# Optimization experiments

Measured on AMD Instinct MI355X. Metric: run time of the kernel, lower is better.

Reference implementation:

```python
import jax, jax.numpy as jnp
import numpy as np

SFREQ = 250.0
L_FREQ, H_FREQ = 4.0, 8.0
N_TAPS = 413  # odd, zero-phase FIR


def _bandpass_fir(numtaps, lf, hf, sfreq):
    # Hamming-windowed sinc band-pass (firwin-style), matching MNE's fir_design='firwin' spirit
    n = np.arange(numtaps) - (numtaps - 1) / 2.0
    lp = lambda fc: (2.0 * fc / sfreq) * np.sinc(2.0 * fc / sfreq * n)
    h = (lp(hf) - lp(lf)) * np.hamming(numtaps)
    return h.astype(np.float32)


def setup_inputs() -> dict:
    key = jax.random.key(0)
    x = jax.random.normal(key, (64, 64, 10000), dtype=jnp.float32)
    h = jnp.asarray(_bandpass_fir(N_TAPS, L_FREQ, H_FREQ, SFREQ))
    return {"x": x, "h": h}


def reference(x, h):
    # x: [B, C, T], h: [n_h] FIR filter. Equivalent math to _overlap_add_filter:
    # reflect_limited padding + full linear FFT convolution + zero-phase crop.
    T = x.shape[-1]
    n_h = h.shape[0]
    n_edge = min(n_h, T) - 1
    # reflect_limited pad: 2*x[0] - x[n_edge:0:-1] (left), 2*x[-1] - x[-2:-n_edge-2:-1] (right)
    left = 2.0 * x[..., :1] - x[..., 1:n_edge + 1][..., ::-1]
    right = 2.0 * x[..., -1:] - x[..., -n_edge - 1:-1][..., ::-1]
    x_ext = jnp.concatenate([left, x, right], axis=-1)  # [B, C, T + 2*n_edge]
    n_x = T + 2 * n_edge
    n_full = n_x + n_h - 1
    n_fft = 1 << (n_full - 1).bit_length()  # single big FFT == overlap-add result
    Xf = jnp.fft.rfft(x_ext, n_fft)
    Hf = jnp.fft.rfft(h.astype(x_ext.dtype), n_fft)
    y = jnp.fft.irfft(Xf * Hf, n_fft)  # full linear convolution of x_ext with h
    shift = (n_h - 1) // 2 + n_edge  # zero-phase delay compensation + edge crop
    return jax.lax.dynamic_slice_in_dim(y, shift, T, axis=-1).astype(x.dtype)
```

## Files before the change

kernel.cpp:

```cpp
#include <hip/hip_runtime.h>


#define T_LEN 10000
#define N_H   413
#define SHIFT 206
#define CB    512
#define NSEG  20
#define ROWH  936
#define NQ    28
#define AROWL 472

typedef _Float16 v8h   __attribute__((ext_vector_type(8)));
typedef float    v16f  __attribute__((ext_vector_type(16)));
typedef float    v4f   __attribute__((ext_vector_type(4)));
typedef float    f32x2 __attribute__((ext_vector_type(2)));

__device__ __forceinline__ void store_col(float* __restrict__ orow, const v16f& acc,
                                          int tbase, int guard_needed) {
    #pragma unroll
    for (int g = 0; g < 4; ++g) {
        if (!guard_needed || (tbase + 8 * g) < T_LEN) {
            *(v4f*)(orow + 8 * g) =
                (v4f){acc[4*g], acc[4*g+1], acc[4*g+2], acc[4*g+3]};
        }
    }
}

__global__ __launch_bounds__(256, 3) void FilterBank_20624432955781_kernel(
    const float* __restrict__ x, const float* __restrict__ h, float* __restrict__ out) {
    __shared__ alignas(16) _Float16 lds_e[16 * ROWH];
    __shared__ alignas(16) _Float16 arow[2][8][AROWL];

    const int tid = threadIdx.x;
    const int t0b = blockIdx.x * CB;
    const int r0  = blockIdx.y * 16;

    for (int z = tid; z < 8 * AROWL; z += 256) {
        const int r = z / AROWL, vv = z - r * AROWL;
        const int idx = 436 + r - vv;
        const float gv = (idx >= 0 && idx < N_H) ? h[idx] : 0.0f;
        const _Float16 hi = (_Float16)gv;
        arow[0][r][vv] = hi;
        arow[1][r][vv] = (_Float16)(gv - (float)hi);
    }

    {
        const int rr = tid >> 4;
        const int jt = tid & 15;
        const float* __restrict__ xr = x + (size_t)(r0 + rr) * T_LEN;
        _Float16* __restrict__ erow = lds_e + rr * ROWH;
        #pragma unroll
        for (int it = 0; it < 4; ++it) {
            const int c = jt + 16 * it;
            if (c < 58) {
                const int j0 = t0b + 16 * c;
                float v[16];
                if (j0 >= SHIFT && j0 + 16 <= T_LEN + SHIFT) {
                    const f32x2* xp = (const f32x2*)(xr + (j0 - SHIFT));
                    #pragma unroll
                    for (int p = 0; p < 8; ++p) { f32x2 t2 = xp[p]; v[2*p] = t2.x; v[2*p+1] = t2.y; }
                } else {
                    #pragma unroll
                    for (int k = 0; k < 16; ++k) {
                        const int j = j0 + k;
                        if (j < SHIFT)              v[k] = 2.0f * xr[0] - xr[SHIFT - j];
                        else if (j < T_LEN + SHIFT) v[k] = xr[j - SHIFT];
                        else                        v[k] = 2.0f * xr[T_LEN - 1] - xr[2 * T_LEN + SHIFT - 2 - j];
                    }
                }
                v8h h0, h1;
                #pragma unroll
                for (int k = 0; k < 8; ++k) { h0[k] = (_Float16)v[k]; h1[k] = (_Float16)v[8 + k]; }
                *(v8h*)(erow + 16 * c)     = h0;
                *(v8h*)(erow + 16 * c + 8) = h1;
            }
        }
    }
    __syncthreads();

    const int l  = tid & 63;
    const int wv = tid >> 6;
    const int n  = l & 31;
    const int hh = l >> 5;
    const int ch = n & 15;
    const int th = n >> 4;
    const int vv0 = 24 + 8 * hh - 8 * (n >> 3);
    const v8h* __restrict__ pah = (const v8h*)(&arow[0][n & 7][0] + vv0);
    const v8h* __restrict__ pal = (const v8h*)(&arow[1][n & 7][0] + vv0);
    const _Float16* __restrict__ ebase = lds_e + ch * ROWH + 32 * th + 8 * hh;

    const int n_out = T_LEN - t0b;
    const int NP = (n_out < CB ? n_out + 63 : CB + 63) >> 6;
    const int guard = (t0b + CB > T_LEN);

    int p = wv;
    if (p + 4 < NP) {
        const _Float16* __restrict__ eb0 = ebase + 64 * p;
        const _Float16* __restrict__ eb1 = ebase + 64 * (p + 4);
        v16f acc0 = (v16f)(0.0f), acc1 = (v16f)(0.0f);
        #pragma unroll
        for (int q = 0; q < NQ; ++q) {
            const v8h ah = pah[2 * q];
            const v8h al = pal[2 * q];
            const v8h b0 = *(const v8h*)(eb0 + 16 * q);
            const v8h b1 = *(const v8h*)(eb1 + 16 * q);
            acc0 = __builtin_amdgcn_mfma_f32_32x32x16_f16(ah, b0, acc0, 0, 0, 0);
            acc1 = __builtin_amdgcn_mfma_f32_32x32x16_f16(ah, b1, acc1, 0, 0, 0);
            acc0 = __builtin_amdgcn_mfma_f32_32x32x16_f16(al, b0, acc0, 0, 0, 0);
            acc1 = __builtin_amdgcn_mfma_f32_32x32x16_f16(al, b1, acc1, 0, 0, 0);
        }
        {
            const int tb0 = t0b + 64 * p + 32 * th + 4 * hh;
            const int tb1 = t0b + 64 * (p + 4) + 32 * th + 4 * hh;
            float* orow = out + (size_t)(r0 + ch) * T_LEN;
            store_col(orow + tb0, acc0, tb0, guard);
            store_col(orow + tb1, acc1, tb1, guard);
        }
        p += 8;
    }
    for (; p < NP; p += 4) {
        const _Float16* __restrict__ eb0 = ebase + 64 * p;
        v16f acc0 = (v16f)(0.0f);
        #pragma unroll
        for (int q = 0; q < NQ; ++q) {
            const v8h ah = pah[2 * q];
            const v8h al = pal[2 * q];
            const v8h b0 = *(const v8h*)(eb0 + 16 * q);
            acc0 = __builtin_amdgcn_mfma_f32_32x32x16_f16(ah, b0, acc0, 0, 0, 0);
            acc0 = __builtin_amdgcn_mfma_f32_32x32x16_f16(al, b0, acc0, 0, 0, 0);
        }
        const int tb0 = t0b + 64 * p + 32 * th + 4 * hh;
        store_col(out + (size_t)(r0 + ch) * T_LEN + tb0, acc0, tb0, guard);
    }
}

extern "C" void kernel_launch(void* const* d_in, const int* in_sizes, int n_in,
                              void* d_out, int out_size, void* d_ws, size_t ws_size,
                              hipStream_t stream) {
    const float* x = (const float*)d_in[0];
    const float* h = (const float*)d_in[1];
    float* out = (float*)d_out;
    dim3 grid(NSEG, 64 * 64 / 16);
    FilterBank_20624432955781_kernel<<<grid, dim3(256), 0, stream>>>(x, h, out);
}
```

Measured before the change: 374.0 us.

## Loop each block over seven segments and prefetch the next input into registers

Each block now processes up to seven consecutive 512-sample segments of its 16 rows instead of one, so the grid shrinks from 20 to 3 column blocks. The fp16 filter Toeplitz table is built once per block instead of once per segment. While the MFMAs run on the current segment, the next segment's input is loaded into registers, then converted and written to LDS between two barriers. MFMA sections also raise wave priority with s_setprio. In exchange there are fewer blocks, more register pressure from the 64-float staging buffer, two extra barriers per segment, and full MFMA work on the partial tail segment.

```diff
diff --git a/kernel.cpp b/kernel.cpp
--- a/kernel.cpp
+++ b/kernel.cpp
@@ -5,7 +5,7 @@
 #define N_H   413
 #define SHIFT 206
 #define CB    512
-#define NSEG  20
+#define BSPAN 3584
 #define ROWH  936
 #define NQ    28
 #define AROWL 472
@@ -14,6 +14,51 @@
 typedef float    v16f  __attribute__((ext_vector_type(16)));
 typedef float    v4f   __attribute__((ext_vector_type(4)));
 typedef float    f32x2 __attribute__((ext_vector_type(2)));
+
+__device__ __forceinline__ void stage_load(const float* __restrict__ xr, int t0s,
+                                           int jt, float sv[4][16]) {
+    #pragma unroll
+    for (int it = 0; it < 4; ++it) {
+        const int c = jt + 16 * it;
+        if (c < 58) {
+            const int j0 = t0s + 16 * c;
+            if (j0 >= SHIFT && j0 + 16 <= T_LEN + SHIFT) {
+                const f32x2* xp = (const f32x2*)(xr + (j0 - SHIFT));
+                #pragma unroll
+                for (int p = 0; p < 8; ++p) {
+                    f32x2 t2 = xp[p]; sv[it][2*p] = t2.x; sv[it][2*p+1] = t2.y;
+                }
+            } else {
+                #pragma unroll
+                for (int k = 0; k < 16; ++k) {
+                    const int j = j0 + k;
+                    float v;
+                    if (j < SHIFT)              v = 2.0f * xr[0] - xr[SHIFT - j];
+                    else if (j < T_LEN + SHIFT) v = xr[j - SHIFT];
+                    else                        v = 2.0f * xr[T_LEN - 1] - xr[2 * T_LEN + SHIFT - 2 - j];
+                    sv[it][k] = v;
+                }
+            }
+        }
+    }
+}
+
+__device__ __forceinline__ void stage_write(_Float16* __restrict__ erow, int jt,
+                                            const float sv[4][16]) {
+    #pragma unroll
+    for (int it = 0; it < 4; ++it) {
+        const int c = jt + 16 * it;
+        if (c < 58) {
+            v8h h0, h1;
+            #pragma unroll
+            for (int k = 0; k < 8; ++k) {
+                h0[k] = (_Float16)sv[it][k]; h1[k] = (_Float16)sv[it][8 + k];
+            }
+            *(v8h*)(erow + 16 * c)     = h0;
+            *(v8h*)(erow + 16 * c + 8) = h1;
+        }
+    }
+}
 
 __device__ __forceinline__ void store_col(float* __restrict__ orow, const v16f& acc,
                                           int tbase, int guard_needed) {
@@ -31,9 +76,10 @@
     __shared__ alignas(16) _Float16 lds_e[16 * ROWH];
     __shared__ alignas(16) _Float16 arow[2][8][AROWL];
 
-    const int tid = threadIdx.x;
-    const int t0b = blockIdx.x * CB;
-    const int r0  = blockIdx.y * 16;
+    const int tid    = threadIdx.x;
+    const int t_base = blockIdx.x * BSPAN;
+    const int r0     = blockIdx.y * 16;
+    const int nseg   = min(7, (T_LEN - t_base + CB - 1) / CB);
 
     for (int z = tid; z < 8 * AROWL; z += 256) {
         const int r = z / AROWL, vv = z - r * AROWL;
@@ -44,38 +90,14 @@
         arow[1][r][vv] = (_Float16)(gv - (float)hi);
     }
 
-    {
-        const int rr = tid >> 4;
-        const int jt = tid & 15;
-        const float* __restrict__ xr = x + (size_t)(r0 + rr) * T_LEN;
-        _Float16* __restrict__ erow = lds_e + rr * ROWH;
-        #pragma unroll
-        for (int it = 0; it < 4; ++it) {
-            const int c = jt + 16 * it;
-            if (c < 58) {
-                const int j0 = t0b + 16 * c;
-                float v[16];
-                if (j0 >= SHIFT && j0 + 16 <= T_LEN + SHIFT) {
-                    const f32x2* xp = (const f32x2*)(xr + (j0 - SHIFT));
-                    #pragma unroll
-                    for (int p = 0; p < 8; ++p) { f32x2 t2 = xp[p]; v[2*p] = t2.x; v[2*p+1] = t2.y; }
-                } else {
-                    #pragma unroll
-                    for (int k = 0; k < 16; ++k) {
-                        const int j = j0 + k;
-                        if (j < SHIFT)              v[k] = 2.0f * xr[0] - xr[SHIFT - j];
-                        else if (j < T_LEN + SHIFT) v[k] = xr[j - SHIFT];
-                        else                        v[k] = 2.0f * xr[T_LEN - 1] - xr[2 * T_LEN + SHIFT - 2 - j];
-                    }
-                }
-                v8h h0, h1;
-                #pragma unroll
-                for (int k = 0; k < 8; ++k) { h0[k] = (_Float16)v[k]; h1[k] = (_Float16)v[8 + k]; }
-                *(v8h*)(erow + 16 * c)     = h0;
-                *(v8h*)(erow + 16 * c + 8) = h1;
-            }
-        }
-    }
+    const int rr = tid >> 4;
+    const int jt = tid & 15;
+    const float* __restrict__ xr = x + (size_t)(r0 + rr) * T_LEN;
+    _Float16* __restrict__ erow = lds_e + rr * ROWH;
+
+    float sv[4][16];
+    stage_load(xr, t_base, jt, sv);
+    stage_write(erow, jt, sv);
     __syncthreads();
 
     const int l  = tid & 63;
@@ -88,15 +110,16 @@
     const v8h* __restrict__ pah = (const v8h*)(&arow[0][n & 7][0] + vv0);
     const v8h* __restrict__ pal = (const v8h*)(&arow[1][n & 7][0] + vv0);
     const _Float16* __restrict__ ebase = lds_e + ch * ROWH + 32 * th + 8 * hh;
+    const _Float16* __restrict__ eb0 = ebase + 64 * wv;
+    const _Float16* __restrict__ eb1 = ebase + 64 * (wv + 4);
+    float* __restrict__ orow = out + (size_t)(r0 + ch) * T_LEN;
 
-    const int n_out = T_LEN - t0b;
-    const int NP = (n_out < CB ? n_out + 63 : CB + 63) >> 6;
-    const int guard = (t0b + CB > T_LEN);
+    for (int s = 0; s < nseg; ++s) {
+        const int t0s = t_base + s * CB;
 
-    int p = wv;
-    if (p + 4 < NP) {
-        const _Float16* __restrict__ eb0 = ebase + 64 * p;
-        const _Float16* __restrict__ eb1 = ebase + 64 * (p + 4);
+        if (s + 1 < nseg) stage_load(xr, t0s + CB, jt, sv);
+
+        __builtin_amdgcn_s_setprio(1);
         v16f acc0 = (v16f)(0.0f), acc1 = (v16f)(0.0f);
         #pragma unroll
         for (int q = 0; q < NQ; ++q) {
@@ -109,28 +132,18 @@
             acc0 = __builtin_amdgcn_mfma_f32_32x32x16_f16(al, b0, acc0, 0, 0, 0);
             acc1 = __builtin_amdgcn_mfma_f32_32x32x16_f16(al, b1, acc1, 0, 0, 0);
         }
-        {
-            const int tb0 = t0b + 64 * p + 32 * th + 4 * hh;
-            const int tb1 = t0b + 64 * (p + 4) + 32 * th + 4 * hh;
-            float* orow = out + (size_t)(r0 + ch) * T_LEN;
-            store_col(orow + tb0, acc0, tb0, guard);
-            store_col(orow + tb1, acc1, tb1, guard);
+        __builtin_amdgcn_s_setprio(0);
+
+        const int guard = (t0s + CB > T_LEN);
+        const int tb0 = t0s + 64 * wv + 32 * th + 4 * hh;
+        store_col(orow + tb0, acc0, tb0, guard);
+        store_col(orow + tb0 + 256, acc1, tb0 + 256, guard);
+
+        if (s + 1 < nseg) {
+            __syncthreads();
+            stage_write(erow, jt, sv);
+            __syncthreads();
         }
-        p += 8;
-    }
-    for (; p < NP; p += 4) {
-        const _Float16* __restrict__ eb0 = ebase + 64 * p;
-        v16f acc0 = (v16f)(0.0f);
-        #pragma unroll
-        for (int q = 0; q < NQ; ++q) {
-            const v8h ah = pah[2 * q];
-            const v8h al = pal[2 * q];
-            const v8h b0 = *(const v8h*)(eb0 + 16 * q);
-            acc0 = __builtin_amdgcn_mfma_f32_32x32x16_f16(ah, b0, acc0, 0, 0, 0);
-            acc0 = __builtin_amdgcn_mfma_f32_32x32x16_f16(al, b0, acc0, 0, 0, 0);
-        }
-        const int tb0 = t0b + 64 * p + 32 * th + 4 * hh;
-        store_col(out + (size_t)(r0 + ch) * T_LEN + tb0, acc0, tb0, guard);
     }
 }
 
@@ -140,6 +153,6 @@
     const float* x = (const float*)d_in[0];
     const float* h = (const float*)d_in[1];
     float* out = (float*)d_out;
-    dim3 grid(NSEG, 64 * 64 / 16);
+    dim3 grid(3, 64 * 64 / 16);
     FilterBank_20624432955781_kernel<<<grid, dim3(256), 0, stream>>>(x, h, out);
 }
```

Measured after the change: 334.5 us. 1.12x faster.
